# Kernel optimization log

Hardware: AMD Instinct MI355X
Metric: run time of the kernel (lower is better)

Reference implementation:

```python
import jax, jax.numpy as jnp
import numpy as np

N = 40000      # nodes
E = 640000     # edges
IN_DIM = 128
HID = 128
HEADS = 4
DHEAD = HID // HEADS  # 32
LAYERS = 3
TIMESTEPS = 2
NEG_SLOPE = 0.2


def setup_inputs() -> dict:
    key = jax.random.key(0)
    ks = jax.random.split(key, 16)
    s = 0.05
    inp = {
        "node_feats": jax.random.normal(ks[0], (N, IN_DIM), jnp.float32),
        "src": jax.random.randint(ks[1], (E,), 0, N, jnp.int32),
        "dst": jax.random.randint(ks[2], (E,), 0, N, jnp.int32),
        "proj_W": jax.random.normal(ks[3], (IN_DIM, HID), jnp.float32) * s,
        "proj_b": jnp.zeros((HID,), jnp.float32),
        "fc_W": jax.random.normal(ks[4], (LAYERS, HID, HID), jnp.float32) * s,
        "attn_l": jax.random.normal(ks[5], (LAYERS, HEADS, DHEAD), jnp.float32) * s,
        "attn_r": jax.random.normal(ks[6], (LAYERS, HEADS, DHEAD), jnp.float32) * s,
        "conv_bias": jnp.zeros((LAYERS, HID), jnp.float32),
        "gru_Wih": jax.random.normal(ks[7], (3 * HID, HID), jnp.float32) * s,
        "gru_Whh": jax.random.normal(ks[8], (3 * HID, HID), jnp.float32) * s,
        "gru_bih": jnp.zeros((3 * HID,), jnp.float32),
        "gru_bhh": jnp.zeros((3 * HID,), jnp.float32),
    }
    return inp


def _gat_layer(h, src, dst, fc_W, attn_l, attn_r, bias):
    # h: (N, HID). DGL GATConv: fc -> edge attn -> segment softmax -> scatter sum
    feat = (h @ fc_W).reshape(N, HEADS, DHEAD)
    el = jnp.einsum('nhd,hd->nh', feat, attn_l)  # (N, H)
    er = jnp.einsum('nhd,hd->nh', feat, attn_r)
    e = jax.nn.leaky_relu(el[src] + er[dst], NEG_SLOPE)  # (E, H)
    # segment softmax over incoming edges per destination node
    emax = jax.ops.segment_max(e, dst, num_segments=N)  # (N, H)
    ee = jnp.exp(e - emax[dst])
    denom = jax.ops.segment_sum(ee, dst, num_segments=N)
    alpha = ee / denom[dst]  # (E, H)
    msg = feat[src] * alpha[:, :, None]  # (E, H, D)
    rst = jax.ops.segment_sum(msg, dst, num_segments=N)  # (N, H, D)
    rst = rst + h.reshape(N, HEADS, DHEAD)          # identity residual
    rst = rst + bias.reshape(HEADS, DHEAD)          # learned bias
    return jax.nn.elu(rst).reshape(N, HID)


def _gru_step(x, Wih, Whh, bih, bhh):
    # seq_len == 1, h0 == 0 -> recurrent matmul Whh @ h0 vanishes; b_hh remains
    gi = x @ Wih.T + bih  # (N, 3*HID)
    r = jax.nn.sigmoid(gi[:, :HID] + bhh[:HID])
    z = jax.nn.sigmoid(gi[:, HID:2 * HID] + bhh[HID:2 * HID])
    n = jnp.tanh(gi[:, 2 * HID:] + r * bhh[2 * HID:])
    return (1.0 - z) * n


def reference(node_feats, src, dst, proj_W, proj_b, fc_W, attn_l, attn_r,
              conv_bias, gru_Wih, gru_Whh, gru_bih, gru_bhh):
    h = node_feats @ proj_W + proj_b
    for l in range(LAYERS):
        h = _gat_layer(h, src, dst, fc_W[l], attn_l[l], attn_r[l], conv_bias[l])
    for _ in range(TIMESTEPS):
        h = _gru_step(h, gru_Wih, gru_Whh, gru_bih, gru_bhh)
    return h
```

## Files before the change

kernel.cpp:

```cpp
#include <hip/hip_runtime.h>
#include <hip/hip_bf16.h>

#define NNODES 40000
#define NEDGES 640000
#define M2PAD  40064
#define HID    128
#define PADCAP 920064
#define WSTRIDE_P (PADCAP + 16)

typedef __attribute__((ext_vector_type(8))) short bf16x8;
typedef __attribute__((ext_vector_type(4))) float f32x4;

__device__ __forceinline__ float bl(unsigned u){ return __uint_as_float(u << 16); }
__device__ __forceinline__ float bh(unsigned u){ return __uint_as_float(u & 0xFFFF0000u); }
__device__ __forceinline__ unsigned short f2b(float f){
    unsigned u = __float_as_uint(f);
    u = (u + 0x7FFFu + ((u >> 16) & 1u)) >> 16;
    return (unsigned short)u;
}
__device__ __forceinline__ float fast_rcp(float x){ return __builtin_amdgcn_rcpf(x); }

__device__ __forceinline__ void g2l16(const void* g, void* l){
    __builtin_amdgcn_global_load_lds(
        (const __attribute__((address_space(1))) unsigned int*)g,
        (__attribute__((address_space(3))) unsigned int*)l, 16, 0, 0);
}

__global__ void prep_all(const float* __restrict__ node_feats,
                         const float* __restrict__ proj_W, const float* __restrict__ fc_W,
                         const float* __restrict__ gru_Wih, const int* __restrict__ dstp,
                         unsigned short* __restrict__ nf,
                         unsigned short* __restrict__ projWT, unsigned short* __restrict__ fcWT,
                         unsigned short* __restrict__ gruWb, int* __restrict__ deg){
    int b = blockIdx.x;
    if (b < 5000){
        int gid = b * 256 + threadIdx.x;
        float4 v = ((const float4*)node_feats)[gid];
        ushort4 o;
        o.x = f2b(v.x); o.y = f2b(v.y); o.z = f2b(v.z); o.w = f2b(v.w);
        ((ushort4*)nf)[gid] = o;
    } else if (b < 5256){
        int t = b - 5000;
        int c = t >> 6;
        int idx = (t & 63) * 256 + threadIdx.x;
        const float* in   = (c == 0) ? proj_W : fc_W + (size_t)(c - 1) * 16384;
        unsigned short* o = (c == 0) ? projWT : fcWT + (size_t)(c - 1) * 16384;
        int k = idx >> 7, n = idx & 127;
        o[n * 128 + k] = f2b(in[idx]);
    } else if (b < 5448){
        int idx = (b - 5256) * 256 + threadIdx.x;
        gruWb[idx] = f2b(gru_Wih[idx]);
    } else {
        int e = (b - 5448) * 256 + threadIdx.x;
        atomicAdd(&deg[dstp[e]], 1);
    }
}

__global__ __launch_bounds__(1024) void scan_kernel(const int* __restrict__ deg,
        int* __restrict__ rowptr, int* __restrict__ cur, int Nn4){
    __shared__ int wsum[17];
    __shared__ int carry;
    int t = threadIdx.x, lane = t & 63, wid = t >> 6;
    if (t == 0) carry = 0;
    __syncthreads();
    for (int base = 0; base < Nn4; base += 1024){
        int i4 = base + t;
        int4 dg = (i4 < Nn4) ? ((const int4*)deg)[i4] : make_int4(0, 0, 0, 0);
        int p0 = (dg.x + 7) & ~7, p1 = (dg.y + 7) & ~7;
        int p2 = (dg.z + 7) & ~7, p3 = (dg.w + 7) & ~7;
        int v = p0 + p1 + p2 + p3;
        int x = v;
        #pragma unroll
        for (int d = 1; d < 64; d <<= 1){
            int y = __shfl_up(x, d, 64);
            if (lane >= d) x += y;
        }
        if (lane == 63) wsum[wid] = x;
        __syncthreads();
        if (wid == 0){
            int vv = (lane < 16) ? wsum[lane] : 0;
            int xx = vv;
            #pragma unroll
            for (int d = 1; d < 16; d <<= 1){
                int y = __shfl_up(xx, d, 64);
                if (lane >= d) xx += y;
            }
            if (lane < 16) wsum[lane] = xx - vv;
            if (lane == 15) wsum[16] = xx;
        }
        __syncthreads();
        int excl = carry + wsum[wid] + (x - v);
        if (i4 < Nn4){
            int4 o = make_int4(excl, excl + p0, excl + p0 + p1, excl + p0 + p1 + p2);
            ((int4*)rowptr)[i4] = o;
            ((int4*)cur)[i4]    = o;
        }
        __syncthreads();
        if (t == 0) carry += wsum[16];
        __syncthreads();
    }
    if (t == 0) rowptr[Nn4 * 4] = carry;
}

__global__ void build_s2n(const int* __restrict__ rowptr, const int* __restrict__ deg,
                          int* __restrict__ s2n){
    int n = blockIdx.x * 256 + threadIdx.x;
    if (n >= NNODES) return;
    int beg = rowptr[n];
    int d   = deg[n];
    for (int p = beg; p < beg + d; p++) s2n[p] = n;
}

__global__ void fill_kernel(const int* __restrict__ src, const int* __restrict__ dst,
                            int* __restrict__ cur, int* __restrict__ esrc){
    int e = blockIdx.x * 256 + threadIdx.x;
    int d = dst[e];
    int pos = atomicAdd(&cur[d], 1);
    esrc[pos] = src[e];
}

template<int MT>
__global__ __launch_bounds__(256) void gemm_t(
        const unsigned short* __restrict__ A, const unsigned short* __restrict__ BT,
        const float* __restrict__ bias, void* __restrict__ C,
        int Mreal, int ldc, int outF32,
        const float* __restrict__ al, const float* __restrict__ ar,
        float* __restrict__ elp, float* __restrict__ erp)
{
    __shared__ unsigned char lds[MT * 256 + 32768];
    unsigned char* ldsA = lds;
    unsigned char* ldsB = lds + MT * 256;
    int w = threadIdx.x >> 6, lane = threadIdx.x & 63;
    int rsub = lane >> 4, c16 = lane & 15;
    long baseM = (long)blockIdx.x * MT;
    long baseN = (long)blockIdx.y * 128;

    #pragma unroll
    for (int i = 0; i < MT / 16; i++){
        int chunk = w * (MT / 16) + i;
        int r = chunk * 4 + rsub;
        int cg = c16 ^ (r & 15);
        long ar_ = baseM + r; if (ar_ >= Mreal) ar_ = Mreal - 1;
        g2l16((const unsigned char*)A + ar_ * 256 + cg * 16, ldsA + chunk * 1024);
    }
    #pragma unroll
    for (int i = 0; i < 8; i++){
        int chunk = w * 8 + i;
        int r = chunk * 4 + rsub;
        int cg = c16 ^ (r & 15);
        long br = baseN + r;
        g2l16((const unsigned char*)BT + br * 256 + cg * 16, ldsB + chunk * 1024);
    }
    __syncthreads();

    constexpr int MI = 4;
    constexpr int NI = (MT == 128) ? 4 : 2;
    int mo = (MT == 128) ? (w & 1) * 64 : 0;
    int no = (MT == 128) ? (w >> 1) * 64 : w * 32;
    int q = lane >> 4, cl = lane & 15;
    f32x4 acc[MI][NI];
    #pragma unroll
    for (int i = 0; i < MI; i++)
        #pragma unroll
        for (int j = 0; j < NI; j++) acc[i][j] = (f32x4){0.f, 0.f, 0.f, 0.f};

    #pragma unroll
    for (int kc = 0; kc < 4; kc++){
        bf16x8 av[MI], bv[NI];
        #pragma unroll
        for (int mi = 0; mi < MI; mi++){
            int row = mo + mi * 16 + cl;
            int cs = (kc * 4 + q) ^ (row & 15);
            av[mi] = *(const bf16x8*)(ldsA + row * 256 + cs * 16);
        }
        #pragma unroll
        for (int ni = 0; ni < NI; ni++){
            int row = no + ni * 16 + cl;
            int cs = (kc * 4 + q) ^ (row & 15);
            bv[ni] = *(const bf16x8*)(ldsB + row * 256 + cs * 16);
        }
        #pragma unroll
        for (int mi = 0; mi < MI; mi++)
            #pragma unroll
            for (int ni = 0; ni < NI; ni++)
                acc[mi][ni] = __builtin_amdgcn_mfma_f32_16x16x32_bf16(av[mi], bv[ni], acc[mi][ni], 0, 0, 0);
    }

    #pragma unroll
    for (int mi = 0; mi < MI; mi++){
        #pragma unroll
        for (int ni = 0; ni < NI; ni++){
            int gn = (int)baseN + no + ni * 16 + cl;
            float bvf = bias ? bias[gn] : 0.f;
            long gm0 = baseM + mo + mi * 16 + q * 4;
            #pragma unroll
            for (int reg = 0; reg < 4; reg++){
                float v = acc[mi][ni][reg] + bvf;
                long gm = gm0 + reg;
                if (gm < Mreal){
                    if (outF32) ((float*)C)[gm * ldc + gn] = v;
                    else ((unsigned short*)C)[gm * ldc + gn] = f2b(v);
                }
            }
        }
    }

    if (NI == 2 && al){
        float al_lo = al[no + cl], al_hi = al[no + 16 + cl];
        float ar_lo = ar[no + cl], ar_hi = ar[no + 16 + cl];
        #pragma unroll
        for (int mi = 0; mi < MI; mi++){
            #pragma unroll
            for (int reg = 0; reg < 4; reg++){
                float pl = acc[mi][0][reg] * al_lo + acc[mi][1][reg] * al_hi;
                float pr = acc[mi][0][reg] * ar_lo + acc[mi][1][reg] * ar_hi;
                #pragma unroll
                for (int msk = 8; msk; msk >>= 1){
                    pl += __shfl_xor(pl, msk, 64);
                    pr += __shfl_xor(pr, msk, 64);
                }
                long gm = baseM + mi * 16 + q * 4 + reg;
                if (cl == 0 && gm < Mreal){
                    elp[gm * 4 + w] = pl;
                    erp[gm * 4 + w] = pr;
                }
            }
        }
    }
}

__global__ __launch_bounds__(256) void gru_fused(
        const unsigned short* __restrict__ A, const unsigned short* __restrict__ BT,
        const float* __restrict__ bih, const float* __restrict__ bhh,
        void* __restrict__ out, int Mreal, int outF32)
{
    __shared__ unsigned char ldsA[16384];
    __shared__ unsigned char ldsB[32768];
    int w = threadIdx.x >> 6, lane = threadIdx.x & 63;
    int rsub = lane >> 4, c16 = lane & 15;
    long baseM = (long)blockIdx.x * 64;

    #pragma unroll
    for (int i = 0; i < 4; i++){
        int chunk = w * 4 + i;
        int r = chunk * 4 + rsub;
        int cg = c16 ^ (r & 15);
        long ar = baseM + r; if (ar >= Mreal) ar = Mreal - 1;
        g2l16((const unsigned char*)A + ar * 256 + cg * 16, ldsA + chunk * 1024);
    }

    int no = w * 32;
    int q = lane >> 4, cl = lane & 15;
    f32x4 acc[3][4][2];
    #pragma unroll
    for (int c = 0; c < 3; c++)
        #pragma unroll
        for (int i = 0; i < 4; i++)
            #pragma unroll
            for (int j = 0; j < 2; j++) acc[c][i][j] = (f32x4){0.f, 0.f, 0.f, 0.f};

    for (int c = 0; c < 3; c++){
        if (c) __syncthreads();
        #pragma unroll
        for (int i = 0; i < 8; i++){
            int chunk = w * 8 + i;
            int r = chunk * 4 + rsub;
            int cg = c16 ^ (r & 15);
            long br = c * 128 + r;
            g2l16((const unsigned char*)BT + br * 256 + cg * 16, ldsB + chunk * 1024);
        }
        __syncthreads();
        #pragma unroll
        for (int kc = 0; kc < 4; kc++){
            bf16x8 av[4], bv[2];
            #pragma unroll
            for (int mi = 0; mi < 4; mi++){
                int row = mi * 16 + cl;
                int cs = (kc * 4 + q) ^ (row & 15);
                av[mi] = *(const bf16x8*)(ldsA + row * 256 + cs * 16);
            }
            #pragma unroll
            for (int ni = 0; ni < 2; ni++){
                int row = no + ni * 16 + cl;
                int cs = (kc * 4 + q) ^ (row & 15);
                bv[ni] = *(const bf16x8*)(ldsB + row * 256 + cs * 16);
            }
            #pragma unroll
            for (int mi = 0; mi < 4; mi++)
                #pragma unroll
                for (int ni = 0; ni < 2; ni++)
                    acc[c][mi][ni] = __builtin_amdgcn_mfma_f32_16x16x32_bf16(av[mi], bv[ni], acc[c][mi][ni], 0, 0, 0);
        }
    }

    #pragma unroll
    for (int ni = 0; ni < 2; ni++){
        int j = no + ni * 16 + cl;
        float bir = bih[j]       + bhh[j];
        float biz = bih[128 + j] + bhh[128 + j];
        float bin = bih[256 + j];
        float bhn = bhh[256 + j];
        #pragma unroll
        for (int mi = 0; mi < 4; mi++){
            long gm0 = baseM + mi * 16 + q * 4;
            #pragma unroll
            for (int reg = 0; reg < 4; reg++){
                long n_row = gm0 + reg;
                float gr = acc[0][mi][ni][reg] + bir;
                float gz = acc[1][mi][ni][reg] + biz;
                float gn = acc[2][mi][ni][reg] + bin;
                float r = fast_rcp(1.f + __expf(-gr));
                float z = fast_rcp(1.f + __expf(-gz));
                float ex = __expf(2.f * (gn + r * bhn));
                float nn = (ex - 1.f) * fast_rcp(ex + 1.f);
                float v = (1.f - z) * nn;
                if (n_row < Mreal){
                    if (outF32) ((float*)out)[n_row * 128 + j] = v;
                    else ((unsigned short*)out)[n_row * 128 + j] = f2b(v);
                }
            }
        }
    }
}

__global__ void edge_w(const int* __restrict__ esrc, const int* __restrict__ s2n,
                       const float* __restrict__ el, const float* __restrict__ er,
                       float* __restrict__ wgtT){
    int p = blockIdx.x * 256 + threadIdx.x;
    int dn = s2n[p];
    if (dn < 0){
        wgtT[0 * WSTRIDE_P + p] = 0.f;
        wgtT[1 * WSTRIDE_P + p] = 0.f;
        wgtT[2 * WSTRIDE_P + p] = 0.f;
        wgtT[3 * WSTRIDE_P + p] = 0.f;
        return;
    }
    int sn = esrc[p];
    float4 l = *(const float4*)(el + (size_t)sn * 4);
    float4 r = *(const float4*)(er + (size_t)dn * 4);
    float e;
    e = l.x + r.x; e = (e > 0.f) ? e : 0.2f * e; wgtT[0 * WSTRIDE_P + p] = __expf(e);
    e = l.y + r.y; e = (e > 0.f) ? e : 0.2f * e; wgtT[1 * WSTRIDE_P + p] = __expf(e);
    e = l.z + r.z; e = (e > 0.f) ? e : 0.2f * e; wgtT[2 * WSTRIDE_P + p] = __expf(e);
    e = l.w + r.w; e = (e > 0.f) ? e : 0.2f * e; wgtT[3 * WSTRIDE_P + p] = __expf(e);
}

__global__ __launch_bounds__(256) void aggregate(
        const int* __restrict__ rowptr, const int* __restrict__ esrc,
        const float* __restrict__ wgtT,
        const unsigned short* __restrict__ feat, const float* __restrict__ bias,
        unsigned short* __restrict__ h)
{
    int wid = threadIdx.x >> 6, lane = threadIdx.x & 63;
    int n = blockIdx.x * 4 + wid;
    int hh = lane >> 4;
    int d0 = lane * 2;
    unsigned doff = (unsigned)(d0 * 2);
    int beg = rowptr[n], end = rowptr[n + 1];
    float s = 0.f, a0 = 0.f, a1 = 0.f;
    const char* fbc = (const char*)feat;
    const float* wp = wgtT + (size_t)hh * WSTRIDE_P + beg;
    const int*   ep = esrc + beg;

    if (beg < end){
        int4 sA = *(const int4*)(ep);
        int4 sB = *(const int4*)(ep + 4);
        float4 wA = make_float4(0.f,0.f,0.f,0.f), wB = wA;
        unsigned f0=0,f1=0,f2=0,f3=0,f4=0,f5=0,f6=0,f7=0;
        for (int p = beg; p < end; p += 8){
            float4 wcA = *(const float4*)(wp);
            float4 wcB = *(const float4*)(wp + 4);
            unsigned c0 = *(const unsigned*)(fbc + ((((unsigned)sA.x) << 8) + doff));
            unsigned c1 = *(const unsigned*)(fbc + ((((unsigned)sA.y) << 8) + doff));
            unsigned c2 = *(const unsigned*)(fbc + ((((unsigned)sA.z) << 8) + doff));
            unsigned c3 = *(const unsigned*)(fbc + ((((unsigned)sA.w) << 8) + doff));
            unsigned c4 = *(const unsigned*)(fbc + ((((unsigned)sB.x) << 8) + doff));
            unsigned c5 = *(const unsigned*)(fbc + ((((unsigned)sB.y) << 8) + doff));
            unsigned c6 = *(const unsigned*)(fbc + ((((unsigned)sB.z) << 8) + doff));
            unsigned c7 = *(const unsigned*)(fbc + ((((unsigned)sB.w) << 8) + doff));
            int4 nA = *(const int4*)(ep + 8);
            int4 nB = *(const int4*)(ep + 12);
            s += ((wA.x + wA.y) + (wA.z + wA.w)) + ((wB.x + wB.y) + (wB.z + wB.w));
            a0 = fmaf(wA.x, bl(f0), fmaf(wA.y, bl(f1), fmaf(wA.z, bl(f2), fmaf(wA.w, bl(f3), a0))));
            a0 = fmaf(wB.x, bl(f4), fmaf(wB.y, bl(f5), fmaf(wB.z, bl(f6), fmaf(wB.w, bl(f7), a0))));
            a1 = fmaf(wA.x, bh(f0), fmaf(wA.y, bh(f1), fmaf(wA.z, bh(f2), fmaf(wA.w, bh(f3), a1))));
            a1 = fmaf(wB.x, bh(f4), fmaf(wB.y, bh(f5), fmaf(wB.z, bh(f6), fmaf(wB.w, bh(f7), a1))));
            wA = wcA; wB = wcB;
            f0 = c0; f1 = c1; f2 = c2; f3 = c3; f4 = c4; f5 = c5; f6 = c6; f7 = c7;
            sA = nA; sB = nB;
            wp += 8; ep += 8;
        }
        s += ((wA.x + wA.y) + (wA.z + wA.w)) + ((wB.x + wB.y) + (wB.z + wB.w));
        a0 = fmaf(wA.x, bl(f0), fmaf(wA.y, bl(f1), fmaf(wA.z, bl(f2), fmaf(wA.w, bl(f3), a0))));
        a0 = fmaf(wB.x, bl(f4), fmaf(wB.y, bl(f5), fmaf(wB.z, bl(f6), fmaf(wB.w, bl(f7), a0))));
        a1 = fmaf(wA.x, bh(f0), fmaf(wA.y, bh(f1), fmaf(wA.z, bh(f2), fmaf(wA.w, bh(f3), a1))));
        a1 = fmaf(wB.x, bh(f4), fmaf(wB.y, bh(f5), fmaf(wB.z, bh(f6), fmaf(wB.w, bh(f7), a1))));
    }
    float inv = (s > 0.f) ? fast_rcp(s) : 0.f;
    unsigned hv = *(const unsigned*)(h + (size_t)n * 128 + d0);
    float x0 = a0 * inv + bl(hv) + bias[d0];
    float x1 = a1 * inv + bh(hv) + bias[d0 + 1];
    x0 = (x0 > 0.f) ? x0 : expm1f(x0);
    x1 = (x1 > 0.f) ? x1 : expm1f(x1);
    unsigned outv = (unsigned)f2b(x0) | ((unsigned)f2b(x1) << 16);
    *(unsigned*)(h + (size_t)n * 128 + d0) = outv;
}

extern "C" void kernel_launch(void* const* d_in, const int* in_sizes, int n_in,
                              void* d_out, int out_size, void* d_ws, size_t ws_size,
                              hipStream_t stream) {
    const float* node_feats = (const float*)d_in[0];
    const int*   srcp       = (const int*)d_in[1];
    const int*   dstp       = (const int*)d_in[2];
    const float* proj_W     = (const float*)d_in[3];
    const float* proj_b     = (const float*)d_in[4];
    const float* fc_W       = (const float*)d_in[5];
    const float* attn_l     = (const float*)d_in[6];
    const float* attn_r     = (const float*)d_in[7];
    const float* conv_bias  = (const float*)d_in[8];
    const float* gru_Wih    = (const float*)d_in[9];
    const float* gru_bih    = (const float*)d_in[11];
    const float* gru_bhh    = (const float*)d_in[12];
    float* outp = (float*)d_out;

    char* ws = (char*)d_ws;
    size_t off = 0;
    auto carve = [&](size_t bytes) -> char* {
        char* p = ws + off;
        off += (bytes + 255) & ~(size_t)255;
        return p;
    };
    int*            deg    = (int*)carve((size_t)NNODES * 4);
    int*            rowptr = (int*)carve((size_t)(NNODES + 1) * 4);
    int*            cur    = (int*)carve((size_t)NNODES * 4);
    int*            esrc   = (int*)carve((size_t)(PADCAP + 32) * 4);
    int*            s2n    = (int*)carve((size_t)PADCAP * 4);
    float*          el     = (float*)carve((size_t)NNODES * 4 * 4);
    float*          er     = (float*)carve((size_t)NNODES * 4 * 4);
    float*          wgtT   = (float*)carve((size_t)4 * WSTRIDE_P * 4);
    unsigned short* projWT = (unsigned short*)carve(16384 * 2);
    unsigned short* fcWT   = (unsigned short*)carve(3 * 16384 * 2);
    unsigned short* gruWb  = (unsigned short*)carve(49152 * 2);
    unsigned short* nf     = (unsigned short*)carve((size_t)NNODES * 128 * 2);
    unsigned short* h      = (unsigned short*)carve((size_t)M2PAD * 128 * 2);
    unsigned short* feat   = (unsigned short*)carve((size_t)M2PAD * 128 * 2);
    (void)ws_size; (void)in_sizes; (void)n_in; (void)out_size;

    hipMemsetAsync(deg, 0, (size_t)NNODES * 4, stream);
    hipMemsetAsync(esrc, 0, (size_t)(PADCAP + 32) * 4, stream);
    hipMemsetAsync(s2n, 0xFF, (size_t)PADCAP * 4, stream);
    prep_all<<<7948, 256, 0, stream>>>(node_feats, proj_W, fc_W, gru_Wih, dstp,
                                       nf, projWT, fcWT, gruWb, deg);
    scan_kernel<<<1, 1024, 0, stream>>>(deg, rowptr, cur, NNODES / 4);
    build_s2n<<<(NNODES + 255) / 256, 256, 0, stream>>>(rowptr, deg, s2n);
    fill_kernel<<<NEDGES / 256, 256, 0, stream>>>(srcp, dstp, cur, esrc);

    gemm_t<64><<<dim3(625, 1), 256, 0, stream>>>(nf, projWT, proj_b, h, NNODES, 128, 0,
                                                 nullptr, nullptr, nullptr, nullptr);

    for (int l = 0; l < 3; l++){
        gemm_t<64><<<dim3(625, 1), 256, 0, stream>>>(h, fcWT + l * 16384, nullptr, feat, NNODES, 128, 0,
                                                     attn_l + l * 128, attn_r + l * 128, el, er);
        edge_w<<<PADCAP / 256, 256, 0, stream>>>(esrc, s2n, el, er, wgtT);
        aggregate<<<NNODES / 4, 256, 0, stream>>>(rowptr, esrc, wgtT, feat, conv_bias + l * 128, h);
    }

    gru_fused<<<625, 256, 0, stream>>>(h, gruWb, gru_bih, gru_bhh, h, NNODES, 0);
    gru_fused<<<625, 256, 0, stream>>>(h, gruWb, gru_bih, gru_bhh, outp, NNODES, 1);
}
```

Before: 367.5 us.

## Process two nodes per wavefront in aggregate and fold memsets into prep kernel

The aggregate kernel now has each wavefront handle two destination nodes with interleaved gather loops, so twice as many independent loads are in flight to hide gather latency. The scan starts with an offset of 8 so that a zero-filled dummy slot exists for the shorter node's padding iterations. The two hipMemsetAsync calls for esrc and s2n are folded into extra blocks of prep_all, removing two launches. The cost is higher register pressure and some wasted work when the two nodes have unbalanced degrees.

```diff
diff --git a/kernel.cpp b/kernel.cpp
--- a/kernel.cpp
+++ b/kernel.cpp
@@ -31,7 +31,8 @@
                          const float* __restrict__ gru_Wih, const int* __restrict__ dstp,
                          unsigned short* __restrict__ nf,
                          unsigned short* __restrict__ projWT, unsigned short* __restrict__ fcWT,
-                         unsigned short* __restrict__ gruWb, int* __restrict__ deg){
+                         unsigned short* __restrict__ gruWb, int* __restrict__ deg,
+                         int* __restrict__ esrc, int* __restrict__ s2n){
     int b = blockIdx.x;
     if (b < 5000){
         int gid = b * 256 + threadIdx.x;
@@ -50,9 +51,15 @@
     } else if (b < 5448){
         int idx = (b - 5256) * 256 + threadIdx.x;
         gruWb[idx] = f2b(gru_Wih[idx]);
-    } else {
+    } else if (b < 7948){
         int e = (b - 5448) * 256 + threadIdx.x;
         atomicAdd(&deg[dstp[e]], 1);
+    } else if (b < 8847){
+        int idx = (b - 7948) * 256 + threadIdx.x;
+        if (idx < (PADCAP + 32) / 4) ((int4*)esrc)[idx] = make_int4(0, 0, 0, 0);
+    } else {
+        int idx = (b - 8847) * 256 + threadIdx.x;
+        if (idx < PADCAP / 4) ((int4*)s2n)[idx] = make_int4(-1, -1, -1, -1);
     }
 }
 
@@ -61,7 +68,7 @@
     __shared__ int wsum[17];
     __shared__ int carry;
     int t = threadIdx.x, lane = t & 63, wid = t >> 6;
-    if (t == 0) carry = 0;
+    if (t == 0) carry = 8;
     __syncthreads();
     for (int base = 0; base < Nn4; base += 1024){
         int i4 = base + t;
@@ -352,58 +359,107 @@
         unsigned short* __restrict__ h)
 {
     int wid = threadIdx.x >> 6, lane = threadIdx.x & 63;
-    int n = blockIdx.x * 4 + wid;
+    int n0 = blockIdx.x * 8 + wid * 2;
     int hh = lane >> 4;
     int d0 = lane * 2;
     unsigned doff = (unsigned)(d0 * 2);
-    int beg = rowptr[n], end = rowptr[n + 1];
-    float s = 0.f, a0 = 0.f, a1 = 0.f;
+    int beg0 = rowptr[n0], mid = rowptr[n0 + 1], end1 = rowptr[n0 + 2];
     const char* fbc = (const char*)feat;
-    const float* wp = wgtT + (size_t)hh * WSTRIDE_P + beg;
-    const int*   ep = esrc + beg;
-
-    if (beg < end){
-        int4 sA = *(const int4*)(ep);
-        int4 sB = *(const int4*)(ep + 4);
-        float4 wA = make_float4(0.f,0.f,0.f,0.f), wB = wA;
-        unsigned f0=0,f1=0,f2=0,f3=0,f4=0,f5=0,f6=0,f7=0;
-        for (int p = beg; p < end; p += 8){
-            float4 wcA = *(const float4*)(wp);
-            float4 wcB = *(const float4*)(wp + 4);
-            unsigned c0 = *(const unsigned*)(fbc + ((((unsigned)sA.x) << 8) + doff));
-            unsigned c1 = *(const unsigned*)(fbc + ((((unsigned)sA.y) << 8) + doff));
-            unsigned c2 = *(const unsigned*)(fbc + ((((unsigned)sA.z) << 8) + doff));
-            unsigned c3 = *(const unsigned*)(fbc + ((((unsigned)sA.w) << 8) + doff));
-            unsigned c4 = *(const unsigned*)(fbc + ((((unsigned)sB.x) << 8) + doff));
-            unsigned c5 = *(const unsigned*)(fbc + ((((unsigned)sB.y) << 8) + doff));
-            unsigned c6 = *(const unsigned*)(fbc + ((((unsigned)sB.z) << 8) + doff));
-            unsigned c7 = *(const unsigned*)(fbc + ((((unsigned)sB.w) << 8) + doff));
-            int4 nA = *(const int4*)(ep + 8);
-            int4 nB = *(const int4*)(ep + 12);
-            s += ((wA.x + wA.y) + (wA.z + wA.w)) + ((wB.x + wB.y) + (wB.z + wB.w));
-            a0 = fmaf(wA.x, bl(f0), fmaf(wA.y, bl(f1), fmaf(wA.z, bl(f2), fmaf(wA.w, bl(f3), a0))));
-            a0 = fmaf(wB.x, bl(f4), fmaf(wB.y, bl(f5), fmaf(wB.z, bl(f6), fmaf(wB.w, bl(f7), a0))));
-            a1 = fmaf(wA.x, bh(f0), fmaf(wA.y, bh(f1), fmaf(wA.z, bh(f2), fmaf(wA.w, bh(f3), a1))));
-            a1 = fmaf(wB.x, bh(f4), fmaf(wB.y, bh(f5), fmaf(wB.z, bh(f6), fmaf(wB.w, bh(f7), a1))));
-            wA = wcA; wB = wcB;
-            f0 = c0; f1 = c1; f2 = c2; f3 = c3; f4 = c4; f5 = c5; f6 = c6; f7 = c7;
-            sA = nA; sB = nB;
-            wp += 8; ep += 8;
-        }
-        s += ((wA.x + wA.y) + (wA.z + wA.w)) + ((wB.x + wB.y) + (wB.z + wB.w));
-        a0 = fmaf(wA.x, bl(f0), fmaf(wA.y, bl(f1), fmaf(wA.z, bl(f2), fmaf(wA.w, bl(f3), a0))));
-        a0 = fmaf(wB.x, bl(f4), fmaf(wB.y, bl(f5), fmaf(wB.z, bl(f6), fmaf(wB.w, bl(f7), a0))));
-        a1 = fmaf(wA.x, bh(f0), fmaf(wA.y, bh(f1), fmaf(wA.z, bh(f2), fmaf(wA.w, bh(f3), a1))));
-        a1 = fmaf(wB.x, bh(f4), fmaf(wB.y, bh(f5), fmaf(wB.z, bh(f6), fmaf(wB.w, bh(f7), a1))));
-    }
-    float inv = (s > 0.f) ? fast_rcp(s) : 0.f;
-    unsigned hv = *(const unsigned*)(h + (size_t)n * 128 + d0);
-    float x0 = a0 * inv + bl(hv) + bias[d0];
-    float x1 = a1 * inv + bh(hv) + bias[d0 + 1];
-    x0 = (x0 > 0.f) ? x0 : expm1f(x0);
-    x1 = (x1 > 0.f) ? x1 : expm1f(x1);
-    unsigned outv = (unsigned)f2b(x0) | ((unsigned)f2b(x1) << 16);
-    *(unsigned*)(h + (size_t)n * 128 + d0) = outv;
+    const float* wz = wgtT + (size_t)hh * WSTRIDE_P;
+
+    int g0 = (mid - beg0) >> 3, g1 = (end1 - mid) >> 3;
+    int iters = (g0 > g1) ? g0 : g1;
+
+    const float* wp0 = (g0 > 0) ? wz + beg0 : wz;
+    const int*   ep0 = (g0 > 0) ? esrc + beg0 : esrc;
+    const float* wp1 = (g1 > 0) ? wz + mid : wz;
+    const int*   ep1 = (g1 > 0) ? esrc + mid : esrc;
+
+    float s0 = 0.f, a00 = 0.f, a01 = 0.f;
+    float s1 = 0.f, a10 = 0.f, a11 = 0.f;
+
+    int4 sA0 = *(const int4*)(ep0);
+    int4 sB0 = *(const int4*)(ep0 + 4);
+    int4 sA1 = *(const int4*)(ep1);
+    int4 sB1 = *(const int4*)(ep1 + 4);
+    float4 wA0 = make_float4(0.f,0.f,0.f,0.f), wB0 = wA0, wA1 = wA0, wB1 = wA0;
+    unsigned p00=0,p01=0,p02=0,p03=0,p04=0,p05=0,p06=0,p07=0;
+    unsigned p10=0,p11=0,p12=0,p13=0,p14=0,p15=0,p16=0,p17=0;
+
+    for (int it = 0; it < iters; it++){
+        float4 wcA0 = *(const float4*)(wp0);
+        float4 wcB0 = *(const float4*)(wp0 + 4);
+        float4 wcA1 = *(const float4*)(wp1);
+        float4 wcB1 = *(const float4*)(wp1 + 4);
+        unsigned c00 = *(const unsigned*)(fbc + ((((unsigned)sA0.x) << 8) + doff));
+        unsigned c01 = *(const unsigned*)(fbc + ((((unsigned)sA0.y) << 8) + doff));
+        unsigned c02 = *(const unsigned*)(fbc + ((((unsigned)sA0.z) << 8) + doff));
+        unsigned c03 = *(const unsigned*)(fbc + ((((unsigned)sA0.w) << 8) + doff));
+        unsigned c04 = *(const unsigned*)(fbc + ((((unsigned)sB0.x) << 8) + doff));
+        unsigned c05 = *(const unsigned*)(fbc + ((((unsigned)sB0.y) << 8) + doff));
+        unsigned c06 = *(const unsigned*)(fbc + ((((unsigned)sB0.z) << 8) + doff));
+        unsigned c07 = *(const unsigned*)(fbc + ((((unsigned)sB0.w) << 8) + doff));
+        unsigned c10 = *(const unsigned*)(fbc + ((((unsigned)sA1.x) << 8) + doff));
+        unsigned c11 = *(const unsigned*)(fbc + ((((unsigned)sA1.y) << 8) + doff));
+        unsigned c12 = *(const unsigned*)(fbc + ((((unsigned)sA1.z) << 8) + doff));
+        unsigned c13 = *(const unsigned*)(fbc + ((((unsigned)sA1.w) << 8) + doff));
+        unsigned c14 = *(const unsigned*)(fbc + ((((unsigned)sB1.x) << 8) + doff));
+        unsigned c15 = *(const unsigned*)(fbc + ((((unsigned)sB1.y) << 8) + doff));
+        unsigned c16_ = *(const unsigned*)(fbc + ((((unsigned)sB1.z) << 8) + doff));
+        unsigned c17 = *(const unsigned*)(fbc + ((((unsigned)sB1.w) << 8) + doff));
+        int4 nA0 = *(const int4*)(ep0 + 8);
+        int4 nB0 = *(const int4*)(ep0 + 12);
+        int4 nA1 = *(const int4*)(ep1 + 8);
+        int4 nB1 = *(const int4*)(ep1 + 12);
+        s0 += ((wA0.x + wA0.y) + (wA0.z + wA0.w)) + ((wB0.x + wB0.y) + (wB0.z + wB0.w));
+        a00 = fmaf(wA0.x, bl(p00), fmaf(wA0.y, bl(p01), fmaf(wA0.z, bl(p02), fmaf(wA0.w, bl(p03), a00))));
+        a00 = fmaf(wB0.x, bl(p04), fmaf(wB0.y, bl(p05), fmaf(wB0.z, bl(p06), fmaf(wB0.w, bl(p07), a00))));
+        a01 = fmaf(wA0.x, bh(p00), fmaf(wA0.y, bh(p01), fmaf(wA0.z, bh(p02), fmaf(wA0.w, bh(p03), a01))));
+        a01 = fmaf(wB0.x, bh(p04), fmaf(wB0.y, bh(p05), fmaf(wB0.z, bh(p06), fmaf(wB0.w, bh(p07), a01))));
+        s1 += ((wA1.x + wA1.y) + (wA1.z + wA1.w)) + ((wB1.x + wB1.y) + (wB1.z + wB1.w));
+        a10 = fmaf(wA1.x, bl(p10), fmaf(wA1.y, bl(p11), fmaf(wA1.z, bl(p12), fmaf(wA1.w, bl(p13), a10))));
+        a10 = fmaf(wB1.x, bl(p14), fmaf(wB1.y, bl(p15), fmaf(wB1.z, bl(p16), fmaf(wB1.w, bl(p17), a10))));
+        a11 = fmaf(wA1.x, bh(p10), fmaf(wA1.y, bh(p11), fmaf(wA1.z, bh(p12), fmaf(wA1.w, bh(p13), a11))));
+        a11 = fmaf(wB1.x, bh(p14), fmaf(wB1.y, bh(p15), fmaf(wB1.z, bh(p16), fmaf(wB1.w, bh(p17), a11))));
+        wA0 = wcA0; wB0 = wcB0; wA1 = wcA1; wB1 = wcB1;
+        p00 = c00; p01 = c01; p02 = c02; p03 = c03; p04 = c04; p05 = c05; p06 = c06; p07 = c07;
+        p10 = c10; p11 = c11; p12 = c12; p13 = c13; p14 = c14; p15 = c15; p16 = c16_; p17 = c17;
+        sA0 = nA0; sB0 = nB0; sA1 = nA1; sB1 = nB1;
+        wp0 += 8; ep0 += 8;
+        wp1 += 8; ep1 += 8;
+        if (it + 1 >= g0) wp0 = wz;
+        if (it + 1 >= g1) wp1 = wz;
+    }
+    s0 += ((wA0.x + wA0.y) + (wA0.z + wA0.w)) + ((wB0.x + wB0.y) + (wB0.z + wB0.w));
+    a00 = fmaf(wA0.x, bl(p00), fmaf(wA0.y, bl(p01), fmaf(wA0.z, bl(p02), fmaf(wA0.w, bl(p03), a00))));
+    a00 = fmaf(wB0.x, bl(p04), fmaf(wB0.y, bl(p05), fmaf(wB0.z, bl(p06), fmaf(wB0.w, bl(p07), a00))));
+    a01 = fmaf(wA0.x, bh(p00), fmaf(wA0.y, bh(p01), fmaf(wA0.z, bh(p02), fmaf(wA0.w, bh(p03), a01))));
+    a01 = fmaf(wB0.x, bh(p04), fmaf(wB0.y, bh(p05), fmaf(wB0.z, bh(p06), fmaf(wB0.w, bh(p07), a01))));
+    s1 += ((wA1.x + wA1.y) + (wA1.z + wA1.w)) + ((wB1.x + wB1.y) + (wB1.z + wB1.w));
+    a10 = fmaf(wA1.x, bl(p10), fmaf(wA1.y, bl(p11), fmaf(wA1.z, bl(p12), fmaf(wA1.w, bl(p13), a10))));
+    a10 = fmaf(wB1.x, bl(p14), fmaf(wB1.y, bl(p15), fmaf(wB1.z, bl(p16), fmaf(wB1.w, bl(p17), a10))));
+    a11 = fmaf(wA1.x, bh(p10), fmaf(wA1.y, bh(p11), fmaf(wA1.z, bh(p12), fmaf(wA1.w, bh(p13), a11))));
+    a11 = fmaf(wB1.x, bh(p14), fmaf(wB1.y, bh(p15), fmaf(wB1.z, bh(p16), fmaf(wB1.w, bh(p17), a11))));
+
+    float bias0 = bias[d0], bias1 = bias[d0 + 1];
+    {
+        float inv = (s0 > 0.f) ? fast_rcp(s0) : 0.f;
+        unsigned hv = *(const unsigned*)(h + (size_t)n0 * 128 + d0);
+        float x0 = a00 * inv + bl(hv) + bias0;
+        float x1 = a01 * inv + bh(hv) + bias1;
+        x0 = (x0 > 0.f) ? x0 : expm1f(x0);
+        x1 = (x1 > 0.f) ? x1 : expm1f(x1);
+        *(unsigned*)(h + (size_t)n0 * 128 + d0) = (unsigned)f2b(x0) | ((unsigned)f2b(x1) << 16);
+    }
+    {
+        float inv = (s1 > 0.f) ? fast_rcp(s1) : 0.f;
+        unsigned hv = *(const unsigned*)(h + (size_t)(n0 + 1) * 128 + d0);
+        float x0 = a10 * inv + bl(hv) + bias0;
+        float x1 = a11 * inv + bh(hv) + bias1;
+        x0 = (x0 > 0.f) ? x0 : expm1f(x0);
+        x1 = (x1 > 0.f) ? x1 : expm1f(x1);
+        *(unsigned*)(h + (size_t)(n0 + 1) * 128 + d0) = (unsigned)f2b(x0) | ((unsigned)f2b(x1) << 16);
+    }
 }
 
 extern "C" void kernel_launch(void* const* d_in, const int* in_sizes, int n_in,
@@ -447,10 +503,8 @@
     (void)ws_size; (void)in_sizes; (void)n_in; (void)out_size;
 
     hipMemsetAsync(deg, 0, (size_t)NNODES * 4, stream);
-    hipMemsetAsync(esrc, 0, (size_t)(PADCAP + 32) * 4, stream);
-    hipMemsetAsync(s2n, 0xFF, (size_t)PADCAP * 4, stream);
-    prep_all<<<7948, 256, 0, stream>>>(node_feats, proj_W, fc_W, gru_Wih, dstp,
-                                       nf, projWT, fcWT, gruWb, deg);
+    prep_all<<<9746, 256, 0, stream>>>(node_feats, proj_W, fc_W, gru_Wih, dstp,
+                                       nf, projWT, fcWT, gruWb, deg, esrc, s2n);
     scan_kernel<<<1, 1024, 0, stream>>>(deg, rowptr, cur, NNODES / 4);
     build_s2n<<<(NNODES + 255) / 256, 256, 0, stream>>>(rowptr, deg, s2n);
     fill_kernel<<<NEDGES / 256, 256, 0, stream>>>(srcp, dstp, cur, esrc);
@@ -462,7 +516,7 @@
         gemm_t<64><<<dim3(625, 1), 256, 0, stream>>>(h, fcWT + l * 16384, nullptr, feat, NNODES, 128, 0,
                                                      attn_l + l * 128, attn_r + l * 128, el, er);
         edge_w<<<PADCAP / 256, 256, 0, stream>>>(esrc, s2n, el, er, wgtT);
-        aggregate<<<NNODES / 4, 256, 0, stream>>>(rowptr, esrc, wgtT, feat, conv_bias + l * 128, h);
+        aggregate<<<NNODES / 8, 256, 0, stream>>>(rowptr, esrc, wgtT, feat, conv_bias + l * 128, h);
     }
 
     gru_fused<<<625, 256, 0, stream>>>(h, gruWb, gru_bih, gru_bhh, h, NNODES, 0);
```

Measured after the change: 369.9 us. Within noise of the previous version (+0.7%).
